# Optimization experiments

Hardware: AMD Instinct MI355X
Metric: run time of the kernel (lower is better)

The kernel has to match this reference:

```python
import jax, jax.numpy as jnp
import numpy as np

T = 4.0          # kd_T
PATCH_NUM = 16
MASK_NUM = 4
P = PATCH_NUM - MASK_NUM  # 12
B = 4096
D_IN = 640
D = 128


def embed(x, w1, b1, w2, b2):
    # Linear -> ReLU -> Linear -> L2 normalize over features
    h = jax.nn.relu(x @ w1.T + b1)
    y = h @ w2.T + b2
    norm = jnp.sqrt(jnp.sum(y * y, axis=1, keepdims=True))
    return y / norm


def kl_rows(y_s, y_t):
    # Matches KLDiv: kl_div(log_softmax(y_s/T), softmax(y_t/T), 'batchmean') * T^2
    # over dim=0 of a 1-D vector -> sum / D. Vectorized over leading dims.
    ls = jax.nn.log_softmax(y_s / T, axis=-1)
    lt = jax.nn.log_softmax(y_t / T, axis=-1)
    pt = jnp.exp(lt)
    return jnp.sum(pt * (lt - ls), axis=-1) / y_s.shape[-1] * (T * T)


def setup_inputs() -> dict:
    key = jax.random.key(0)
    ks = jax.random.split(key, 11)
    return {
        "ebg": jax.random.normal(ks[0], (B, D_IN), jnp.float32),
        "ebp": jax.random.normal(ks[1], (P * B, D_IN), jnp.float32),
        "labelsg": jax.random.randint(ks[2], (B,), 0, 64),
        "glo_w1": jax.random.normal(ks[3], (D, D_IN), jnp.float32) * 0.04,
        "glo_b1": jax.random.normal(ks[4], (D,), jnp.float32) * 0.02,
        "glo_w2": jax.random.normal(ks[5], (D, D), jnp.float32) * 0.09,
        "glo_b2": jax.random.normal(ks[6], (D,), jnp.float32) * 0.02,
        "pat_w1": jax.random.normal(ks[7], (D, D_IN), jnp.float32) * 0.04,
        "pat_b1": jax.random.normal(ks[8], (D,), jnp.float32) * 0.02,
        "pat_w2": jax.random.normal(ks[9], (D, D), jnp.float32) * 0.09,
        "pat_b2": jax.random.normal(ks[10], (D,), jnp.float32) * 0.02,
    }


def reference(ebg, ebp, labelsg, glo_w1, glo_b1, glo_w2, glo_b2,
              pat_w1, pat_b1, pat_w2, pat_b2):
    sg = jax.lax.stop_gradient
    g = embed(ebg, glo_w1, glo_b1, glo_w2, glo_b2)          # [B, D]
    p = embed(ebp, pat_w1, pat_b1, pat_w2, pat_b2)          # [P*B, D]
    p = p.reshape(P, B, D)
    p_bar = p.mean(axis=0)                                  # [B, D]

    # soft_dil_loss: symmetric KL between g[b] and p_bar[b]
    dil = jnp.sum(kl_rows(g, sg(p_bar)) + kl_rows(p_bar, sg(g)))

    # soft_dcl_loss: symmetric KL between (g[b]-p[b,l])^2 and (p_bar[b]-p[b,l])^2
    p_bt = jnp.transpose(p, (1, 0, 2))                      # [B, P, D]
    d1 = (g[:, None, :] - p_bt) ** 2                        # [B, P, D]
    d2 = (p_bar[:, None, :] - p_bt) ** 2                    # [B, P, D]
    dcl = jnp.sum(kl_rows(d1, sg(d2)) + kl_rows(d2, sg(d1))) / P

    return (dil, dcl)
```

## Files before the change

kernel.cpp:

```cpp
#include <hip/hip_runtime.h>
#include <math.h>

#define B_    4096
#define DIN   640
#define DD    128
#define PP    12
#define INV_T 0.25f

typedef __bf16 bft;
typedef __attribute__((ext_vector_type(8))) __bf16 bf16x8;
typedef __attribute__((ext_vector_type(4))) float fx4;

__global__ __launch_bounds__(256) void prep_kernel(
    const float* __restrict__ gw1, const float* __restrict__ pw1,
    const float* __restrict__ gw2, const float* __restrict__ pw2,
    bft* __restrict__ w1hg, bft* __restrict__ w1lg,
    bft* __restrict__ w1hp, bft* __restrict__ w1lp,
    bft* __restrict__ w2hg, bft* __restrict__ w2lg,
    bft* __restrict__ w2hp, bft* __restrict__ w2lp)
{
  int idx = blockIdx.x * 256 + threadIdx.x;
  const float* src; bft *dh, *dl; int off;
  if (idx < 81920)       { src = gw1; dh = w1hg; dl = w1lg; off = idx; }
  else if (idx < 163840) { src = pw1; dh = w1hp; dl = w1lp; off = idx - 81920; }
  else if (idx < 180224) { src = gw2; dh = w2hg; dl = w2lg; off = idx - 163840; }
  else                   { src = pw2; dh = w2hp; dl = w2lp; off = idx - 180224; }
  float x = src[off];
  bft h = (bft)x;
  dh[off] = h;
  dl[off] = (bft)(x - (float)h);
}

__global__ __launch_bounds__(256, 2) void embed_kernel(
    const float* __restrict__ ebg, const float* __restrict__ ebp,
    const bft* __restrict__ w1hg, const bft* __restrict__ w1lg, const float* __restrict__ b1g,
    const bft* __restrict__ w2hg, const bft* __restrict__ w2lg, const float* __restrict__ b2g,
    const bft* __restrict__ w1hp, const bft* __restrict__ w1lp, const float* __restrict__ b1p,
    const bft* __restrict__ w2hp, const bft* __restrict__ w2lp, const float* __restrict__ b2p,
    float* __restrict__ outg, float* __restrict__ outp)
{
  __shared__ bft hsm[2 * 128 * 128];
  bft* hhi = hsm;
  bft* hlo = hsm + 128 * 128;
  float* halfsq = (float*)hsm;

  const int t = threadIdx.x;
  const int w = t >> 6, lane = t & 63;
  const int wm = w >> 1, wn = w & 1;
  const int ln = lane & 15, quad = lane >> 4;

  const float *X, *B1, *B2;
  const bft *W1H, *W1L, *W2H, *W2L;
  float* Y;
  long m0;
  if (blockIdx.x < 32) {
    X = ebg; W1H = w1hg; W1L = w1lg; B1 = b1g; W2H = w2hg; W2L = w2lg; B2 = b2g;
    Y = outg; m0 = (long)blockIdx.x * 128;
  } else {
    X = ebp; W1H = w1hp; W1L = w1lp; B1 = b1p; W2H = w2hp; W2L = w2lp; B2 = b2p;
    Y = outp; m0 = (long)(blockIdx.x - 32) * 128;
  }

  const float* xptr[4];
  const bft *p1h[4], *p1l[4];
#pragma unroll
  for (int mt = 0; mt < 4; mt++)
    xptr[mt] = X + (size_t)(m0 + wm * 64 + mt * 16 + ln) * DIN + quad * 8;
#pragma unroll
  for (int nt = 0; nt < 4; nt++) {
    int n = wn * 64 + nt * 16 + ln;
    p1h[nt] = W1H + (size_t)n * DIN + quad * 8;
    p1l[nt] = W1L + (size_t)n * DIN + quad * 8;
  }

  fx4 acc[4][4];
#pragma unroll
  for (int mt = 0; mt < 4; mt++)
#pragma unroll
    for (int nt = 0; nt < 4; nt++) acc[mt][nt] = (fx4){0.f, 0.f, 0.f, 0.f};

#define LOADX(dst, koff)                                   \
  _Pragma("unroll")                                        \
  for (int mt = 0; mt < 4; mt++) {                         \
    dst[mt][0] = *(const fx4*)(xptr[mt] + (koff));         \
    dst[mt][1] = *(const fx4*)(xptr[mt] + (koff) + 4);     \
  }

#define CONVX(src, ah, al)                                 \
  _Pragma("unroll")                                        \
  for (int mt = 0; mt < 4; mt++)                           \
    _Pragma("unroll")                                      \
    for (int q = 0; q < 2; q++)                            \
      _Pragma("unroll")                                    \
      for (int j = 0; j < 4; j++) {                        \
        float xv = src[mt][q][j];                          \
        bft hh = (bft)xv;                                  \
        ah[mt][q * 4 + j] = hh;                            \
        al[mt][q * 4 + j] = (bft)(xv - (float)hh);         \
      }

#define MFMA3(ah, al, k0)                                                              \
  {                                                                                    \
    bf16x8 bh[4], bl[4];                                                               \
    _Pragma("unroll")                                                                  \
    for (int nt = 0; nt < 4; nt++) {                                                   \
      bh[nt] = *(const bf16x8*)(p1h[nt] + (k0));                                       \
      bl[nt] = *(const bf16x8*)(p1l[nt] + (k0));                                       \
    }                                                                                  \
    _Pragma("unroll")                                                                  \
    for (int mt = 0; mt < 4; mt++)                                                     \
      _Pragma("unroll")                                                                \
      for (int nt = 0; nt < 4; nt++) {                                                 \
        acc[mt][nt] = __builtin_amdgcn_mfma_f32_16x16x32_bf16(ah[mt], bh[nt], acc[mt][nt], 0, 0, 0); \
        acc[mt][nt] = __builtin_amdgcn_mfma_f32_16x16x32_bf16(al[mt], bh[nt], acc[mt][nt], 0, 0, 0); \
        acc[mt][nt] = __builtin_amdgcn_mfma_f32_16x16x32_bf16(ah[mt], bl[nt], acc[mt][nt], 0, 0, 0); \
      }                                                                                \
  }

  fx4 xa[4][2], xb[4][2];
  bf16x8 ah[4], al[4];
  LOADX(xa, 0)
  for (int kc = 0; kc < 20; kc += 2) {
    const int k0 = kc * 32;
    LOADX(xb, k0 + 32)
    CONVX(xa, ah, al)
    MFMA3(ah, al, k0)
    if (kc < 18) { LOADX(xa, k0 + 64) }
    CONVX(xb, ah, al)
    MFMA3(ah, al, k0 + 32)
  }

#pragma unroll
  for (int nt = 0; nt < 4; nt++) {
    float bv = B1[wn * 64 + nt * 16 + ln];
    int c8 = wn * 8 + nt * 2 + (ln >> 3);
    int c7 = ln & 7;
#pragma unroll
    for (int mt = 0; mt < 4; mt++) {
#pragma unroll
      for (int r = 0; r < 4; r++) {
        float v = fmaxf(acc[mt][nt][r] + bv, 0.f);
        bft h = (bft)v;
        bft l = (bft)(v - (float)h);
        int m = wm * 64 + mt * 16 + quad * 4 + r;
        int addr = m * 128 + ((c8 ^ (m & 15)) << 3) + c7;
        hhi[addr] = h;
        hlo[addr] = l;
      }
    }
  }
  __syncthreads();

  fx4 acc2[4][4];
#pragma unroll
  for (int nt = 0; nt < 4; nt++) {
    float bv = B2[wn * 64 + nt * 16 + ln];
#pragma unroll
    for (int mt = 0; mt < 4; mt++) acc2[mt][nt] = (fx4){bv, bv, bv, bv};
  }
  const bft *p2h[4], *p2l[4];
#pragma unroll
  for (int nt = 0; nt < 4; nt++) {
    int n = wn * 64 + nt * 16 + ln;
    p2h[nt] = W2H + (size_t)n * DD + quad * 8;
    p2l[nt] = W2L + (size_t)n * DD + quad * 8;
  }
#pragma unroll
  for (int kc = 0; kc < 4; kc++) {
    const int k0 = kc * 32;
    bf16x8 bh2[4], bl2[4], ah2[4], al2[4];
#pragma unroll
    for (int nt = 0; nt < 4; nt++) {
      bh2[nt] = *(const bf16x8*)(p2h[nt] + k0);
      bl2[nt] = *(const bf16x8*)(p2l[nt] + k0);
    }
#pragma unroll
    for (int mt = 0; mt < 4; mt++) {
      int m = wm * 64 + mt * 16 + ln;
      int c8 = (kc * 4 + quad) ^ (m & 15);
      ah2[mt] = *(const bf16x8*)&hhi[m * 128 + (c8 << 3)];
      al2[mt] = *(const bf16x8*)&hlo[m * 128 + (c8 << 3)];
    }
#pragma unroll
    for (int mt = 0; mt < 4; mt++)
#pragma unroll
      for (int nt = 0; nt < 4; nt++) {
        acc2[mt][nt] = __builtin_amdgcn_mfma_f32_16x16x32_bf16(ah2[mt], bh2[nt], acc2[mt][nt], 0, 0, 0);
        acc2[mt][nt] = __builtin_amdgcn_mfma_f32_16x16x32_bf16(al2[mt], bh2[nt], acc2[mt][nt], 0, 0, 0);
        acc2[mt][nt] = __builtin_amdgcn_mfma_f32_16x16x32_bf16(ah2[mt], bl2[nt], acc2[mt][nt], 0, 0, 0);
      }
  }
  __syncthreads();

#pragma unroll
  for (int mt = 0; mt < 4; mt++) {
#pragma unroll
    for (int r = 0; r < 4; r++) {
      float s = 0.f;
#pragma unroll
      for (int nt = 0; nt < 4; nt++) { float v = acc2[mt][nt][r]; s += v * v; }
      s += __shfl_xor(s, 1, 64);
      s += __shfl_xor(s, 2, 64);
      s += __shfl_xor(s, 4, 64);
      s += __shfl_xor(s, 8, 64);
      if (ln == 0) halfsq[(wm * 64 + mt * 16 + quad * 4 + r) * 2 + wn] = s;
    }
  }
  __syncthreads();
#pragma unroll
  for (int mt = 0; mt < 4; mt++) {
#pragma unroll
    for (int r = 0; r < 4; r++) {
      int row = wm * 64 + mt * 16 + quad * 4 + r;
      float rinv = 1.0f / sqrtf(halfsq[row * 2] + halfsq[row * 2 + 1]);
#pragma unroll
      for (int nt = 0; nt < 4; nt++)
        Y[(m0 + row) * DD + wn * 64 + nt * 16 + ln] = acc2[mt][nt][r] * rinv;
    }
  }
}

__device__ __forceinline__ float sym_kl_row(float au0, float au1, float av0, float av1)
{
  float mu = fmaxf(au0, au1);
  float mv = fmaxf(av0, av1);
#pragma unroll
  for (int o = 32; o > 0; o >>= 1) {
    mu = fmaxf(mu, __shfl_xor(mu, o, 64));
    mv = fmaxf(mv, __shfl_xor(mv, o, 64));
  }
  float eu0 = expf(au0 - mu), eu1 = expf(au1 - mu);
  float ev0 = expf(av0 - mv), ev1 = expf(av1 - mv);
  float su = eu0 + eu1, sv = ev0 + ev1;
#pragma unroll
  for (int o = 32; o > 0; o >>= 1) {
    su += __shfl_xor(su, o, 64);
    sv += __shfl_xor(sv, o, 64);
  }
  float ru = 1.0f / su, rv = 1.0f / sv;
  float d0 = au0 - av0, d1 = au1 - av1;
  float part = (eu0 * ru - ev0 * rv) * d0 + (eu1 * ru - ev1 * rv) * d1;
#pragma unroll
  for (int o = 32; o > 0; o >>= 1) part += __shfl_xor(part, o, 64);
  return part;
}

__global__ __launch_bounds__(256) void loss_kernel(
    const float* __restrict__ g, const float* __restrict__ p,
    float* __restrict__ pdil, float* __restrict__ pdcl)
{
  __shared__ float wd[4], wc[4];
  int w = threadIdx.x >> 6, lane = threadIdx.x & 63;
  int b = blockIdx.x * 4 + w;
  float2 pl[PP];
  float sx = 0.f, sy = 0.f;
#pragma unroll
  for (int l = 0; l < PP; l++) {
    pl[l] = *(const float2*)&p[((size_t)l * B_ + b) * DD + lane * 2];
    sx += pl[l].x; sy += pl[l].y;
  }
  sx *= (1.0f / PP); sy *= (1.0f / PP);
  float2 gv = *(const float2*)&g[(size_t)b * DD + lane * 2];

  float dil = sym_kl_row(gv.x * INV_T, gv.y * INV_T, sx * INV_T, sy * INV_T) * 0.125f;

  float dcl = 0.f;
#pragma unroll
  for (int l = 0; l < PP; l++) {
    float u0 = (gv.x - pl[l].x) * (gv.x - pl[l].x) * INV_T;
    float u1 = (gv.y - pl[l].y) * (gv.y - pl[l].y) * INV_T;
    float v0 = (sx - pl[l].x) * (sx - pl[l].x) * INV_T;
    float v1 = (sy - pl[l].y) * (sy - pl[l].y) * INV_T;
    dcl += sym_kl_row(u0, u1, v0, v1);
  }
  dcl *= (1.0f / 96.0f);

  if (lane == 0) { wd[w] = dil; wc[w] = dcl; }
  __syncthreads();
  if (threadIdx.x == 0) pdil[blockIdx.x] = wd[0] + wd[1] + wd[2] + wd[3];
  if (threadIdx.x == 1) pdcl[blockIdx.x] = wc[0] + wc[1] + wc[2] + wc[3];
}

__global__ __launch_bounds__(256) void final_kernel(const float* __restrict__ pdil,
                                                    const float* __restrict__ pdcl,
                                                    float* __restrict__ out)
{
  __shared__ float red[8];
  int t = threadIdx.x;
  float s0 = 0.f, s1 = 0.f;
  for (int i = t; i < 1024; i += 256) { s0 += pdil[i]; s1 += pdcl[i]; }
#pragma unroll
  for (int o = 32; o > 0; o >>= 1) {
    s0 += __shfl_xor(s0, o, 64);
    s1 += __shfl_xor(s1, o, 64);
  }
  int wid = t >> 6, lane = t & 63;
  if (lane == 0) { red[wid] = s0; red[4 + wid] = s1; }
  __syncthreads();
  if (t == 0) out[0] = red[0] + red[1] + red[2] + red[3];
  if (t == 1) out[1] = red[4] + red[5] + red[6] + red[7];
}

extern "C" void kernel_launch(void* const* d_in, const int* in_sizes, int n_in,
                              void* d_out, int out_size, void* d_ws, size_t ws_size,
                              hipStream_t stream)
{
  const float* ebg = (const float*)d_in[0];
  const float* ebp = (const float*)d_in[1];
  const float* gw1 = (const float*)d_in[3];
  const float* gb1 = (const float*)d_in[4];
  const float* gw2 = (const float*)d_in[5];
  const float* gb2 = (const float*)d_in[6];
  const float* pw1 = (const float*)d_in[7];
  const float* pb1 = (const float*)d_in[8];
  const float* pw2 = (const float*)d_in[9];
  const float* pb2 = (const float*)d_in[10];
  float* out = (float*)d_out;

  float* ws   = (float*)d_ws;
  float* g    = ws;
  float* p    = g + (size_t)B_ * DD;
  float* pdil = p + (size_t)PP * B_ * DD;
  float* pdcl = pdil + 1024;
  bft* wb     = (bft*)(pdcl + 1024);
  bft* w1hg = wb;                 bft* w1lg = w1hg + 81920;
  bft* w1hp = w1lg + 81920;       bft* w1lp = w1hp + 81920;
  bft* w2hg = w1lp + 81920;       bft* w2lg = w2hg + 16384;
  bft* w2hp = w2lg + 16384;       bft* w2lp = w2hp + 16384;

  prep_kernel<<<768, 256, 0, stream>>>(gw1, pw1, gw2, pw2,
                                       w1hg, w1lg, w1hp, w1lp,
                                       w2hg, w2lg, w2hp, w2lp);
  embed_kernel<<<416, 256, 0, stream>>>(ebg, ebp,
                                        w1hg, w1lg, gb1, w2hg, w2lg, gb2,
                                        w1hp, w1lp, pb1, w2hp, w2lp, pb2,
                                        g, p);
  loss_kernel<<<B_ / 4, 256, 0, stream>>>(g, p, pdil, pdcl);
  final_kernel<<<1, 256, 0, stream>>>(pdil, pdcl, out);
}
```

Baseline: 294.2 us.

## Double-buffer weight loads in both GEMM phases and drop softmax max reduction

Phase-1 weight fragments are now prefetched one chunk ahead alongside the X loads, instead of being loaded right before their MFMAs. Phase-2 weight loads are issued before the barrier and ping-ponged across chunks, so global latency overlaps the LDS barrier and MFMA work. In the KL helper, the max-subtraction shuffle reductions are removed and fast __expf is used. This is safe only because inputs are bounded: L2-normalized vectors scaled by 1/T, or squared differences of them. It costs extra registers, which may reduce occupancy.

```diff
diff --git a/kernel.cpp b/kernel.cpp
--- a/kernel.cpp
+++ b/kernel.cpp
@@ -84,6 +84,13 @@
   for (int mt = 0; mt < 4; mt++) {                         \
     dst[mt][0] = *(const fx4*)(xptr[mt] + (koff));         \
     dst[mt][1] = *(const fx4*)(xptr[mt] + (koff) + 4);     \
+  }
+
+#define LOADW(wh, wl, koff)                                \
+  _Pragma("unroll")                                        \
+  for (int nt = 0; nt < 4; nt++) {                         \
+    wh[nt] = *(const bf16x8*)(p1h[nt] + (koff));           \
+    wl[nt] = *(const bf16x8*)(p1l[nt] + (koff));           \
   }
 
 #define CONVX(src, ah, al)                                 \
@@ -99,35 +106,33 @@
         al[mt][q * 4 + j] = (bft)(xv - (float)hh);         \
       }
 
-#define MFMA3(ah, al, k0)                                                              \
-  {                                                                                    \
-    bf16x8 bh[4], bl[4];                                                               \
+#define MFMA3R(ah, al, wh, wl)                                                         \
+  _Pragma("unroll")                                                                    \
+  for (int mt = 0; mt < 4; mt++)                                                       \
     _Pragma("unroll")                                                                  \
     for (int nt = 0; nt < 4; nt++) {                                                   \
-      bh[nt] = *(const bf16x8*)(p1h[nt] + (k0));                                       \
-      bl[nt] = *(const bf16x8*)(p1l[nt] + (k0));                                       \
-    }                                                                                  \
-    _Pragma("unroll")                                                                  \
-    for (int mt = 0; mt < 4; mt++)                                                     \
-      _Pragma("unroll")                                                                \
-      for (int nt = 0; nt < 4; nt++) {                                                 \
-        acc[mt][nt] = __builtin_amdgcn_mfma_f32_16x16x32_bf16(ah[mt], bh[nt], acc[mt][nt], 0, 0, 0); \
-        acc[mt][nt] = __builtin_amdgcn_mfma_f32_16x16x32_bf16(al[mt], bh[nt], acc[mt][nt], 0, 0, 0); \
-        acc[mt][nt] = __builtin_amdgcn_mfma_f32_16x16x32_bf16(ah[mt], bl[nt], acc[mt][nt], 0, 0, 0); \
-      }                                                                                \
-  }
+      acc[mt][nt] = __builtin_amdgcn_mfma_f32_16x16x32_bf16(ah[mt], wh[nt], acc[mt][nt], 0, 0, 0); \
+      acc[mt][nt] = __builtin_amdgcn_mfma_f32_16x16x32_bf16(al[mt], wh[nt], acc[mt][nt], 0, 0, 0); \
+      acc[mt][nt] = __builtin_amdgcn_mfma_f32_16x16x32_bf16(ah[mt], wl[nt], acc[mt][nt], 0, 0, 0); \
+    }
 
   fx4 xa[4][2], xb[4][2];
   bf16x8 ah[4], al[4];
+  bf16x8 wha[4], wla[4], whb[4], wlb[4];
   LOADX(xa, 0)
+  LOADW(wha, wla, 0)
   for (int kc = 0; kc < 20; kc += 2) {
     const int k0 = kc * 32;
     LOADX(xb, k0 + 32)
+    LOADW(whb, wlb, k0 + 32)
     CONVX(xa, ah, al)
-    MFMA3(ah, al, k0)
-    if (kc < 18) { LOADX(xa, k0 + 64) }
+    MFMA3R(ah, al, wha, wla)
+    if (kc < 18) {
+      LOADX(xa, k0 + 64)
+      LOADW(wha, wla, k0 + 64)
+    }
     CONVX(xb, ah, al)
-    MFMA3(ah, al, k0 + 32)
+    MFMA3R(ah, al, whb, wlb)
   }
 
 #pragma unroll
@@ -149,15 +154,7 @@
       }
     }
   }
-  __syncthreads();
-
-  fx4 acc2[4][4];
-#pragma unroll
-  for (int nt = 0; nt < 4; nt++) {
-    float bv = B2[wn * 64 + nt * 16 + ln];
-#pragma unroll
-    for (int mt = 0; mt < 4; mt++) acc2[mt][nt] = (fx4){bv, bv, bv, bv};
-  }
+
   const bft *p2h[4], *p2l[4];
 #pragma unroll
   for (int nt = 0; nt < 4; nt++) {
@@ -165,31 +162,51 @@
     p2h[nt] = W2H + (size_t)n * DD + quad * 8;
     p2l[nt] = W2L + (size_t)n * DD + quad * 8;
   }
-#pragma unroll
-  for (int kc = 0; kc < 4; kc++) {
-    const int k0 = kc * 32;
-    bf16x8 bh2[4], bl2[4], ah2[4], al2[4];
-#pragma unroll
-    for (int nt = 0; nt < 4; nt++) {
-      bh2[nt] = *(const bf16x8*)(p2h[nt] + k0);
-      bl2[nt] = *(const bf16x8*)(p2l[nt] + k0);
-    }
-#pragma unroll
-    for (int mt = 0; mt < 4; mt++) {
-      int m = wm * 64 + mt * 16 + ln;
-      int c8 = (kc * 4 + quad) ^ (m & 15);
-      ah2[mt] = *(const bf16x8*)&hhi[m * 128 + (c8 << 3)];
-      al2[mt] = *(const bf16x8*)&hlo[m * 128 + (c8 << 3)];
-    }
-#pragma unroll
-    for (int mt = 0; mt < 4; mt++)
-#pragma unroll
-      for (int nt = 0; nt < 4; nt++) {
-        acc2[mt][nt] = __builtin_amdgcn_mfma_f32_16x16x32_bf16(ah2[mt], bh2[nt], acc2[mt][nt], 0, 0, 0);
-        acc2[mt][nt] = __builtin_amdgcn_mfma_f32_16x16x32_bf16(al2[mt], bh2[nt], acc2[mt][nt], 0, 0, 0);
-        acc2[mt][nt] = __builtin_amdgcn_mfma_f32_16x16x32_bf16(ah2[mt], bl2[nt], acc2[mt][nt], 0, 0, 0);
-      }
-  }
+  fx4 acc2[4][4];
+#pragma unroll
+  for (int nt = 0; nt < 4; nt++) {
+    float bv = B2[wn * 64 + nt * 16 + ln];
+#pragma unroll
+    for (int mt = 0; mt < 4; mt++) acc2[mt][nt] = (fx4){bv, bv, bv, bv};
+  }
+
+#define LOADW2(wh, wl, koff)                               \
+  _Pragma("unroll")                                        \
+  for (int nt = 0; nt < 4; nt++) {                         \
+    wh[nt] = *(const bf16x8*)(p2h[nt] + (koff));           \
+    wl[nt] = *(const bf16x8*)(p2l[nt] + (koff));           \
+  }
+
+#define PH2CHUNK(kcv, wh, wl)                                                          \
+  {                                                                                    \
+    bf16x8 ah2[4], al2[4];                                                             \
+    _Pragma("unroll")                                                                  \
+    for (int mt = 0; mt < 4; mt++) {                                                   \
+      int m = wm * 64 + mt * 16 + ln;                                                  \
+      int c8 = ((kcv) * 4 + quad) ^ (m & 15);                                          \
+      ah2[mt] = *(const bf16x8*)&hhi[m * 128 + (c8 << 3)];                             \
+      al2[mt] = *(const bf16x8*)&hlo[m * 128 + (c8 << 3)];                             \
+    }                                                                                  \
+    _Pragma("unroll")                                                                  \
+    for (int mt = 0; mt < 4; mt++)                                                     \
+      _Pragma("unroll")                                                                \
+      for (int nt = 0; nt < 4; nt++) {                                                 \
+        acc2[mt][nt] = __builtin_amdgcn_mfma_f32_16x16x32_bf16(ah2[mt], wh[nt], acc2[mt][nt], 0, 0, 0); \
+        acc2[mt][nt] = __builtin_amdgcn_mfma_f32_16x16x32_bf16(al2[mt], wh[nt], acc2[mt][nt], 0, 0, 0); \
+        acc2[mt][nt] = __builtin_amdgcn_mfma_f32_16x16x32_bf16(ah2[mt], wl[nt], acc2[mt][nt], 0, 0, 0); \
+      }                                                                                \
+  }
+
+  bf16x8 q2ha[4], q2la[4], q2hb[4], q2lb[4];
+  LOADW2(q2ha, q2la, 0)
+  __syncthreads();
+  LOADW2(q2hb, q2lb, 32)
+  PH2CHUNK(0, q2ha, q2la)
+  LOADW2(q2ha, q2la, 64)
+  PH2CHUNK(1, q2hb, q2lb)
+  LOADW2(q2hb, q2lb, 96)
+  PH2CHUNK(2, q2ha, q2la)
+  PH2CHUNK(3, q2hb, q2lb)
   __syncthreads();
 
 #pragma unroll
@@ -222,15 +239,8 @@
 
 __device__ __forceinline__ float sym_kl_row(float au0, float au1, float av0, float av1)
 {
-  float mu = fmaxf(au0, au1);
-  float mv = fmaxf(av0, av1);
-#pragma unroll
-  for (int o = 32; o > 0; o >>= 1) {
-    mu = fmaxf(mu, __shfl_xor(mu, o, 64));
-    mv = fmaxf(mv, __shfl_xor(mv, o, 64));
-  }
-  float eu0 = expf(au0 - mu), eu1 = expf(au1 - mu);
-  float ev0 = expf(av0 - mv), ev1 = expf(av1 - mv);
+  float eu0 = __expf(au0), eu1 = __expf(au1);
+  float ev0 = __expf(av0), ev1 = __expf(av1);
   float su = eu0 + eu1, sv = ev0 + ev1;
 #pragma unroll
   for (int o = 32; o > 0; o >>= 1) {
```

Result: no change. 294.2 us (+0.0%).
